# Performance work log

Hardware: AMD Instinct MI355X
Metric: run time of the kernel (lower is better)

## Reference

```python
import jax, jax.numpy as jnp
import numpy as np

B, T, D, L, E = 8, 2048, 256, 8, 64


def setup_inputs() -> dict:
    key = jax.random.key(0)
    ks = jax.random.split(key, 5)
    x = jax.random.normal(ks[0], (B, T, D), dtype=jnp.float32)
    # MMLP params: weight (4L, D, E), bias (4L, E); nn.Linear: (2L, D), (2L,)
    W_ml = jax.random.normal(ks[1], (4 * L, D, E), dtype=jnp.float32) * 0.05
    b_ml = jax.random.normal(ks[2], (4 * L, E), dtype=jnp.float32) * 0.05
    W_lin = jax.random.normal(ks[3], (2 * L, D), dtype=jnp.float32) * 0.05
    b_lin = jax.random.normal(ks[4], (2 * L,), dtype=jnp.float32) * 0.05
    return {"x": x, "W_ml": W_ml, "b_ml": b_ml, "W_lin": W_lin, "b_lin": b_lin}


def _xlstm_forward(x, W_ml, b_ml, W_lin, b_lin):
    b, t, _ = x.shape
    l4, _, e = W_ml.shape
    l = l4 // 4
    # Precompute all per-step gate projections at once (the torch code does this per step).
    mg = jnp.einsum('bti,lij->btlj', x, W_ml) + b_ml          # (B,T,4L,E)
    lg = jnp.einsum('bti,li->btl', x, W_lin) + b_lin          # (B,T,2L)
    o_, v, k, q = jnp.split(mg, 4, axis=2)                    # each (B,T,L,E)
    i_, f_ = jnp.split(lg, 2, axis=2)                         # each (B,T,L)
    xs = tuple(jnp.moveaxis(a, 1, 0) for a in (o_, v, k, q, i_, f_))  # time-major

    def step(carry, inp):
        m, n, C, h = carry
        o_t, v_t, k_t, q_t, i_t, f_t = inp
        m_new = jnp.maximum(f_t + m, i_t)                     # stabilizer (B,L)
        i_g = jnp.exp(i_t - m_new)
        f_g = jnp.exp(f_t + m - m_new)
        # rank-1 outer-product update of matrix cell state (B,L,E,E)
        C = f_g[:, :, None, None] * C + i_g[:, :, None, None] * (v_t[:, :, :, None] * k_t[:, :, None, :])
        n = f_g[:, :, None] * n + i_g[:, :, None] * k_t       # (B,L,E)
        denom = jnp.maximum(jnp.sum(n * q_t, axis=-1), 1.0)[:, :, None]  # clamp(.,1,inf)
        h = jax.nn.sigmoid(o_t) * jnp.einsum('blij,bli->blj', C, q_t) / denom
        return (m_new, n, C, h), None

    init = (
        jnp.zeros((b, l), jnp.float32),
        jnp.zeros((b, l, e), jnp.float32),
        jnp.zeros((b, l, e, e), jnp.float32),
        jnp.zeros((b, l, e), jnp.float32),
    )
    (m, n, C, h), _ = jax.lax.scan(step, init, xs)
    return h, C


def reference(x, W_ml, b_ml, W_lin, b_lin):
    return _xlstm_forward(x, W_ml, b_ml, W_lin, b_lin)
```

## Files before the change

### kernel.cpp

```cpp
#include <hip/hip_runtime.h>

#define B 8
#define T 2048
#define D 256
#define L 8
#define E 64
#define BT (B*T)

typedef _Float16 f16;
typedef f16 f16x8 __attribute__((ext_vector_type(8)));
typedef float f32x4 __attribute__((ext_vector_type(4)));

#define OFF_I   0
#define OFF_F   (OFF_I  + B*L*T)
#define OFF_W16 (OFF_F  + B*L*T)
#define OFF_WT  (OFF_W16 + B*L*T/2)
#define OFF_VT  (OFF_WT + 16*E*D/2)
#define OFF_KT  (OFF_VT + B*L*E*T/2)
#define OFF_CP  (OFF_KT + B*L*E*T/2)
#define OFF_X16 (OFF_CP + 64*4*4160)

__global__ __launch_bounds__(256) void k_prep_x(const float* __restrict__ x,
                                                f16* __restrict__ x16) {
    int i = (blockIdx.x * 256 + threadIdx.x) * 8;
    float4 v0 = *(const float4*)(x + i);
    float4 v1 = *(const float4*)(x + i + 4);
    f16x8 o;
    o[0] = (f16)v0.x; o[1] = (f16)v0.y; o[2] = (f16)v0.z; o[3] = (f16)v0.w;
    o[4] = (f16)v1.x; o[5] = (f16)v1.y; o[6] = (f16)v1.z; o[7] = (f16)v1.w;
    *(f16x8*)(x16 + i) = o;
}

__global__ __launch_bounds__(256) void k_prep(const float* __restrict__ x,
        const float* __restrict__ Wlin, const float* __restrict__ blin,
        const float* __restrict__ Wml,
        float* __restrict__ ibuf, float* __restrict__ fbuf,
        f16* __restrict__ Wt16) {
    __shared__ __align__(16) char smem[49920];
    int tid = threadIdx.x;
    int bx = blockIdx.x;
    if (bx < 512) {
        float (*xs)[260] = (float(*)[260])smem;
        float (*wsm)[260] = (float(*)[260])(smem + 33280);
        int t0 = bx * 32;
        {
            int row = tid >> 3, q = tid & 7;
            const float* src = x + (size_t)(t0 + row) * D + q * 32;
            #pragma unroll
            for (int j = 0; j < 8; ++j) {
                float4 v = *(const float4*)(src + j * 4);
                *(float4*)&xs[row][q * 32 + j * 4] = v;
            }
        }
        {
            int row = tid >> 4, c0 = (tid & 15) * 16;
            const float* src = Wlin + row * D + c0;
            #pragma unroll
            for (int j = 0; j < 4; ++j) {
                float4 v = *(const float4*)(src + j * 4);
                *(float4*)&wsm[row][c0 + j * 4] = v;
            }
        }
        __syncthreads();
        int tl = tid >> 4, g = tid & 15;
        float acc0 = 0.f, acc1 = 0.f;
        for (int i = 0; i < D; ++i) {
            float wv = wsm[g][i];
            acc0 += xs[tl * 2 + 0][i] * wv;
            acc1 += xs[tl * 2 + 1][i] * wv;
        }
        float bias = blin[g];
        float acc[2] = {acc0 + bias, acc1 + bias};
        #pragma unroll
        for (int u = 0; u < 2; ++u) {
            int t = t0 + tl * 2 + u;
            int b = t >> 11, tt = t & 2047;
            if (g < 8) ibuf[(b * L + g) * T + tt] = acc[u];
            else       fbuf[(b * L + (g - 8)) * T + tt] = acc[u];
        }
    } else {
        float (*ts)[65] = (float(*)[65])smem;
        int vkrow = bx - 512;
        int wrow = 8 + vkrow;
        for (int dc = 0; dc < 4; ++dc) {
            int d0 = dc * 64;
            int r = tid >> 2, cq = (tid & 3) * 16;
            const float* src = Wml + ((size_t)wrow * D + d0 + r) * E + cq;
            #pragma unroll
            for (int j = 0; j < 16; j += 4) {
                float4 v = *(const float4*)(src + j);
                ts[r][cq + j] = v.x; ts[r][cq + j + 1] = v.y;
                ts[r][cq + j + 2] = v.z; ts[r][cq + j + 3] = v.w;
            }
            __syncthreads();
            int e = tid >> 2, dq = (tid & 3) * 16;
            f16* dst = Wt16 + ((size_t)vkrow * E + e) * D + d0 + dq;
            f16x8 o0, o1;
            #pragma unroll
            for (int j = 0; j < 8; ++j) {
                o0[j] = (f16)ts[dq + j][e];
                o1[j] = (f16)ts[dq + 8 + j][e];
            }
            *(f16x8*)dst = o0;
            *(f16x8*)(dst + 8) = o1;
            __syncthreads();
        }
    }
}

__global__ __launch_bounds__(256) void k_scan(const float* __restrict__ ibuf,
        const float* __restrict__ fbuf, f16* __restrict__ w16) {
    __shared__ float part[256];
    __shared__ float red[256];
    int tid = threadIdx.x;
    int base = blockIdx.x * T;
    const float* fp = fbuf + base + tid * 8;
    const float* ip = ibuf + base + tid * 8;
    float4 fa = *(const float4*)fp;
    float4 fb = *(const float4*)(fp + 4);
    float4 ia = *(const float4*)ip;
    float4 ib = *(const float4*)(ip + 4);
    float f[8] = {fa.x, fa.y, fa.z, fa.w, fb.x, fb.y, fb.z, fb.w};
    float iv[8] = {ia.x, ia.y, ia.z, ia.w, ib.x, ib.y, ib.z, ib.w};
    float ls[8]; float run = 0.f;
    #pragma unroll
    for (int r = 0; r < 8; ++r) { run += f[r]; ls[r] = run; }
    part[tid] = run;
    __syncthreads();
    float inc = run;
    #pragma unroll
    for (int s = 1; s < 256; s <<= 1) {
        float u = (tid >= s) ? part[tid - s] : 0.f;
        __syncthreads();
        inc += u;
        part[tid] = inc;
        __syncthreads();
    }
    float off = inc - run;
    float e[8]; float lmax = -1e30f;
    #pragma unroll
    for (int r = 0; r < 8; ++r) { e[r] = iv[r] - (off + ls[r]); lmax = fmaxf(lmax, e[r]); }
    red[tid] = lmax;
    __syncthreads();
    for (int s = 128; s > 0; s >>= 1) {
        if (tid < s) red[tid] = fmaxf(red[tid], red[tid + s]);
        __syncthreads();
    }
    float M = fmaxf(red[0], 0.0f);
    f16x8 wv8;
    #pragma unroll
    for (int r = 0; r < 8; ++r) wv8[r] = (f16)__expf(e[r] - M);
    *(f16x8*)(w16 + base + tid * 8) = wv8;
}

__global__ __launch_bounds__(512) void k_vkproj3(const f16* __restrict__ x16,
        const f16* __restrict__ Wt16, const float* __restrict__ bml,
        f16* __restrict__ Vt, f16* __restrict__ Kt) {
    __shared__ __align__(16) char lds[40960];
    int tid = threadIdx.x;
    int bx = blockIdx.x, h = blockIdx.y;
    int t0 = bx * 128;
    const f16* xa = x16 + (size_t)t0 * D;
    const f16* wb = Wt16 + (size_t)h * 8 * E * D;
    int wv = tid >> 6, lane = tid & 63;
    int wr = wv >> 2, wc = wv & 3;
    int q = lane >> 4, lr = lane & 15;
    int sa_t = tid >> 2, sa_q = tid & 3;
    f32x4 acc[4][8] = {};
    for (int ks = 0; ks < 8; ++ks) {
        int k0 = ks * 32;
        {
            f16x8 v = *(const f16x8*)(xa + (size_t)sa_t * D + k0 + sa_q * 8);
            int ba = sa_t * 64 + ((sa_q ^ ((sa_t >> 1) & 3)) << 4);
            *(f16x8*)(lds + ba) = v;
        }
        #pragma unroll
        for (int rr = 0; rr < 4; ++rr) {
            int r = rr * 128 + (tid >> 2);
            int c = tid & 3;
            f16x8 v = *(const f16x8*)(wb + (size_t)r * D + k0 + c * 8);
            int ba = 8192 + r * 64 + ((c ^ ((r >> 1) & 3)) << 4);
            *(f16x8*)(lds + ba) = v;
        }
        __syncthreads();
        f16x8 a[4], bf[8];
        #pragma unroll
        for (int m = 0; m < 4; ++m) {
            int t = wr * 64 + m * 16 + lr;
            int ba = t * 64 + ((q ^ ((t >> 1) & 3)) << 4);
            a[m] = *(const f16x8*)(lds + ba);
        }
        #pragma unroll
        for (int n = 0; n < 8; ++n) {
            int c = wc * 128 + n * 16 + lr;
            int ba = 8192 + c * 64 + ((q ^ ((c >> 1) & 3)) << 4);
            bf[n] = *(const f16x8*)(lds + ba);
        }
        #pragma unroll
        for (int m = 0; m < 4; ++m)
            #pragma unroll
            for (int n = 0; n < 8; ++n)
                acc[m][n] = __builtin_amdgcn_mfma_f32_16x16x32_f16(
                    a[m], bf[n], acc[m][n], 0, 0, 0);
        __syncthreads();
    }
    const float* bp = bml + (size_t)(8 + h * 8) * E;
    int b_g = t0 >> 11, tin = t0 & 2047;
    f16* obase = h ? Kt : Vt;
    for (int p = 0; p < 4; ++p) {
        if (wc == p) {
            #pragma unroll
            for (int n = 0; n < 8; ++n) {
                int cc = n * 16 + lr;
                float bias = bp[p * 128 + cc];
                int swz = (cc & 7) << 4;
                #pragma unroll
                for (int m = 0; m < 4; ++m) {
                    #pragma unroll
                    for (int r = 0; r < 4; r += 2) {
                        int t = wr * 64 + m * 16 + q * 4 + r;
                        union { f16 h2[2]; unsigned u; } pk;
                        pk.h2[0] = (f16)(acc[m][n][r] + bias);
                        pk.h2[1] = (f16)(acc[m][n][r + 1] + bias);
                        int ba = cc * 256 + ((t * 2) ^ swz);
                        *(unsigned*)(lds + ba) = pk.u;
                    }
                }
            }
        }
        __syncthreads();
        {
            int cc = tid >> 2, part = tid & 3;
            int cg = p * 128 + cc;
            int l = cg >> 6, e = cg & 63;
            f16* dst = obase + ((size_t)((b_g * L + l) * E + e)) * T + tin + part * 32;
            int swz = (cc & 7) << 4;
            #pragma unroll
            for (int jj = 0; jj < 4; ++jj) {
                int t = part * 32 + jj * 8;
                int ba = cc * 256 + ((t * 2) ^ swz);
                *(f16x8*)(dst + jj * 8) = *(const f16x8*)(lds + ba);
            }
        }
        __syncthreads();
    }
}

__global__ __launch_bounds__(256) void k_cgemm2(const f16* __restrict__ Vt,
        const f16* __restrict__ Kt, const f16* __restrict__ w16,
        float* __restrict__ Cpart) {
    __shared__ float red[64 * 64];
    __shared__ float redn[64];
    int tid = threadIdx.x;
    int bl = blockIdx.x, tc = blockIdx.y;
    int wv = tid >> 6, lane = tid & 63;
    const f16* vp = Vt + (size_t)bl * E * T;
    const f16* kp = Kt + (size_t)bl * E * T;
    const f16* wp = w16 + (size_t)bl * T;
    f32x4 acc[5][4] = {};
    int tbase = tc * 512 + wv * 128;
    for (int kc = 0; kc < 4; ++kc) {
        int tt = tbase + kc * 32 + (lane >> 4) * 8;
        f16x8 wfrag = *(const f16x8*)(wp + tt);
        f16x8 a[5], bf[4];
        #pragma unroll
        for (int m = 0; m < 4; ++m) {
            int i = m * 16 + (lane & 15);
            f16x8 v = *(const f16x8*)(vp + (size_t)i * T + tt);
            a[m] = v * wfrag;
        }
        a[4] = wfrag;
        #pragma unroll
        for (int nn = 0; nn < 4; ++nn) {
            int j = nn * 16 + (lane & 15);
            bf[nn] = *(const f16x8*)(kp + (size_t)j * T + tt);
        }
        #pragma unroll
        for (int m = 0; m < 5; ++m)
            #pragma unroll
            for (int nn = 0; nn < 4; ++nn)
                acc[m][nn] = __builtin_amdgcn_mfma_f32_16x16x32_f16(
                    a[m], bf[nn], acc[m][nn], 0, 0, 0);
    }
    for (int rr = 0; rr < 4; ++rr) {
        if (wv == rr) {
            #pragma unroll
            for (int m = 0; m < 4; ++m)
                #pragma unroll
                for (int nn = 0; nn < 4; ++nn)
                    #pragma unroll
                    for (int r = 0; r < 4; ++r) {
                        int row = m * 16 + (lane >> 4) * 4 + r;
                        int col = nn * 16 + (lane & 15);
                        if (rr == 0) red[row * 64 + col] = acc[m][nn][r];
                        else         red[row * 64 + col] += acc[m][nn][r];
                    }
            if ((lane >> 4) == 0) {
                #pragma unroll
                for (int nn = 0; nn < 4; ++nn) {
                    int col = nn * 16 + (lane & 15);
                    if (rr == 0) redn[col] = acc[4][nn][0];
                    else         redn[col] += acc[4][nn][0];
                }
            }
        }
        __syncthreads();
    }
    float* cp = Cpart + ((size_t)bl * 4 + tc) * 4160;
    #pragma unroll
    for (int j = 0; j < 4; ++j) {
        int idx = tid * 16 + j * 4;
        *(float4*)(cp + idx) = *(const float4*)(red + idx);
    }
    if (tid < 64) cp[4096 + tid] = redn[tid];
}

__global__ __launch_bounds__(256) void k_final(const float* __restrict__ x,
        const float* __restrict__ Wml, const float* __restrict__ bml,
        const float* __restrict__ Cpart, float* __restrict__ out) {
    __shared__ float Cs[E * E];
    __shared__ float xs[D];
    __shared__ float ns[E];
    __shared__ float os[E];
    __shared__ float qs[E];
    int tid = threadIdx.x;
    int bl = blockIdx.x; int b = bl >> 3, l = bl & 7;
    xs[tid] = x[((size_t)(b * T + (T - 1))) * D + tid];
    const float* cp = Cpart + (size_t)bl * 4 * 4160;
    #pragma unroll
    for (int j = 0; j < 4; ++j) {
        int idx = tid * 16 + j * 4;
        float4 s = {0, 0, 0, 0};
        #pragma unroll
        for (int p = 0; p < 4; ++p) {
            float4 v = *(const float4*)(cp + p * 4160 + idx);
            s.x += v.x; s.y += v.y; s.z += v.z; s.w += v.w;
        }
        *(float4*)&Cs[idx] = s;
        *(float4*)(out + 4096 + (size_t)bl * (E * E) + idx) = s;
    }
    if (tid < 64) {
        float s = 0.f;
        #pragma unroll
        for (int p = 0; p < 4; ++p) s += cp[p * 4160 + 4096 + tid];
        ns[tid] = s;
    }
    __syncthreads();
    if (tid < 128) {
        int gate = tid >> 6, e = tid & 63;
        int wrow = gate ? (3 * L + l) : l;
        const float* wpp = Wml + (size_t)wrow * D * E + e;
        float s = 0.f;
        for (int kk = 0; kk < D; ++kk) s += xs[kk] * wpp[kk * E];
        s += bml[wrow * E + e];
        if (gate) qs[e] = s; else os[e] = s;
    }
    __syncthreads();
    if (tid < 64) {
        int j = tid;
        float hc = 0.f;
        for (int i2 = 0; i2 < E; ++i2) hc += Cs[i2 * E + j] * qs[i2];
        float nq = 0.f;
        for (int i2 = 0; i2 < E; ++i2) nq += ns[i2] * qs[i2];
        float denom = fmaxf(nq, 1.0f);
        float sg = 1.0f / (1.0f + __expf(-os[j]));
        out[bl * E + j] = sg * hc / denom;
    }
}

extern "C" void kernel_launch(void* const* d_in, const int* in_sizes, int n_in,
                              void* d_out, int out_size, void* d_ws, size_t ws_size,
                              hipStream_t stream) {
    const float* x    = (const float*)d_in[0];
    const float* Wml  = (const float*)d_in[1];
    const float* bml  = (const float*)d_in[2];
    const float* Wlin = (const float*)d_in[3];
    const float* blin = (const float*)d_in[4];
    float* out = (float*)d_out;
    float* ws = (float*)d_ws;
    float* ibuf  = ws + OFF_I;
    float* fbuf  = ws + OFF_F;
    f16*   w16   = (f16*)(ws + OFF_W16);
    f16*   Wt16  = (f16*)(ws + OFF_WT);
    f16*   Vt    = (f16*)(ws + OFF_VT);
    f16*   Kt    = (f16*)(ws + OFF_KT);
    float* Cpart = ws + OFF_CP;
    f16*   x16   = (f16*)(ws + OFF_X16);

    k_prep_x<<<BT * D / (256 * 8), 256, 0, stream>>>(x, x16);
    k_prep<<<512 + 16, 256, 0, stream>>>(x, Wlin, blin, Wml, ibuf, fbuf, Wt16);
    k_scan<<<B * L, 256, 0, stream>>>(ibuf, fbuf, w16);
    k_vkproj3<<<dim3(BT / 128, 2), 512, 0, stream>>>(x16, Wt16, bml, Vt, Kt);
    k_cgemm2<<<dim3(B * L, 4), 256, 0, stream>>>(Vt, Kt, w16, Cpart);
    k_final<<<B * L, 256, 0, stream>>>(x, Wml, bml, Cpart, out);
}
```

Measured before the change: 71.39 us.

## Fuse x conversion into prep kernel and gate scan into C-GEMM kernel

Merges the fp32-to-fp16 conversion of x into the prep kernel as extra blocks, and folds the log-space gate scan into the C-GEMM kernel, where each block recomputes the prefix sum and max for its (b,l) row and keeps its slice of weights in LDS. This removes two kernel launches and the global round trip of the weight buffer. In exchange, the scan is computed redundantly by the four time-chunk blocks of each row, and its barrier-heavy prologue now sits in front of the MFMA loop.

Result: faster. 65.34 us, median of 3 (-8.5%).

```diff
diff --git a/kernel.cpp b/kernel.cpp
--- a/kernel.cpp
+++ b/kernel.cpp
@@ -13,29 +13,17 @@
 
 #define OFF_I   0
 #define OFF_F   (OFF_I  + B*L*T)
-#define OFF_W16 (OFF_F  + B*L*T)
-#define OFF_WT  (OFF_W16 + B*L*T/2)
+#define OFF_WT  (OFF_F  + B*L*T)
 #define OFF_VT  (OFF_WT + 16*E*D/2)
 #define OFF_KT  (OFF_VT + B*L*E*T/2)
 #define OFF_CP  (OFF_KT + B*L*E*T/2)
 #define OFF_X16 (OFF_CP + 64*4*4160)
 
-__global__ __launch_bounds__(256) void k_prep_x(const float* __restrict__ x,
-                                                f16* __restrict__ x16) {
-    int i = (blockIdx.x * 256 + threadIdx.x) * 8;
-    float4 v0 = *(const float4*)(x + i);
-    float4 v1 = *(const float4*)(x + i + 4);
-    f16x8 o;
-    o[0] = (f16)v0.x; o[1] = (f16)v0.y; o[2] = (f16)v0.z; o[3] = (f16)v0.w;
-    o[4] = (f16)v1.x; o[5] = (f16)v1.y; o[6] = (f16)v1.z; o[7] = (f16)v1.w;
-    *(f16x8*)(x16 + i) = o;
-}
-
-__global__ __launch_bounds__(256) void k_prep(const float* __restrict__ x,
+__global__ __launch_bounds__(256) void k_prep_all(const float* __restrict__ x,
         const float* __restrict__ Wlin, const float* __restrict__ blin,
         const float* __restrict__ Wml,
         float* __restrict__ ibuf, float* __restrict__ fbuf,
-        f16* __restrict__ Wt16) {
+        f16* __restrict__ Wt16, f16* __restrict__ x16) {
     __shared__ __align__(16) char smem[49920];
     int tid = threadIdx.x;
     int bx = blockIdx.x;
@@ -78,7 +66,7 @@
             if (g < 8) ibuf[(b * L + g) * T + tt] = acc[u];
             else       fbuf[(b * L + (g - 8)) * T + tt] = acc[u];
         }
-    } else {
+    } else if (bx < 528) {
         float (*ts)[65] = (float(*)[65])smem;
         int vkrow = bx - 512;
         int wrow = 8 + vkrow;
@@ -105,52 +93,15 @@
             *(f16x8*)(dst + 8) = o1;
             __syncthreads();
         }
-    }
-}
-
-__global__ __launch_bounds__(256) void k_scan(const float* __restrict__ ibuf,
-        const float* __restrict__ fbuf, f16* __restrict__ w16) {
-    __shared__ float part[256];
-    __shared__ float red[256];
-    int tid = threadIdx.x;
-    int base = blockIdx.x * T;
-    const float* fp = fbuf + base + tid * 8;
-    const float* ip = ibuf + base + tid * 8;
-    float4 fa = *(const float4*)fp;
-    float4 fb = *(const float4*)(fp + 4);
-    float4 ia = *(const float4*)ip;
-    float4 ib = *(const float4*)(ip + 4);
-    float f[8] = {fa.x, fa.y, fa.z, fa.w, fb.x, fb.y, fb.z, fb.w};
-    float iv[8] = {ia.x, ia.y, ia.z, ia.w, ib.x, ib.y, ib.z, ib.w};
-    float ls[8]; float run = 0.f;
-    #pragma unroll
-    for (int r = 0; r < 8; ++r) { run += f[r]; ls[r] = run; }
-    part[tid] = run;
-    __syncthreads();
-    float inc = run;
-    #pragma unroll
-    for (int s = 1; s < 256; s <<= 1) {
-        float u = (tid >= s) ? part[tid - s] : 0.f;
-        __syncthreads();
-        inc += u;
-        part[tid] = inc;
-        __syncthreads();
-    }
-    float off = inc - run;
-    float e[8]; float lmax = -1e30f;
-    #pragma unroll
-    for (int r = 0; r < 8; ++r) { e[r] = iv[r] - (off + ls[r]); lmax = fmaxf(lmax, e[r]); }
-    red[tid] = lmax;
-    __syncthreads();
-    for (int s = 128; s > 0; s >>= 1) {
-        if (tid < s) red[tid] = fmaxf(red[tid], red[tid + s]);
-        __syncthreads();
-    }
-    float M = fmaxf(red[0], 0.0f);
-    f16x8 wv8;
-    #pragma unroll
-    for (int r = 0; r < 8; ++r) wv8[r] = (f16)__expf(e[r] - M);
-    *(f16x8*)(w16 + base + tid * 8) = wv8;
+    } else {
+        int i = ((bx - 528) * 256 + tid) * 8;
+        float4 v0 = *(const float4*)(x + i);
+        float4 v1 = *(const float4*)(x + i + 4);
+        f16x8 o;
+        o[0] = (f16)v0.x; o[1] = (f16)v0.y; o[2] = (f16)v0.z; o[3] = (f16)v0.w;
+        o[4] = (f16)v1.x; o[5] = (f16)v1.y; o[6] = (f16)v1.z; o[7] = (f16)v1.w;
+        *(f16x8*)(x16 + i) = o;
+    }
 }
 
 __global__ __launch_bounds__(512) void k_vkproj3(const f16* __restrict__ x16,
@@ -246,22 +197,67 @@
     }
 }
 
-__global__ __launch_bounds__(256) void k_cgemm2(const f16* __restrict__ Vt,
-        const f16* __restrict__ Kt, const f16* __restrict__ w16,
-        float* __restrict__ Cpart) {
+__global__ __launch_bounds__(256) void k_cgemm2s(const f16* __restrict__ Vt,
+        const f16* __restrict__ Kt, const float* __restrict__ ibuf,
+        const float* __restrict__ fbuf, float* __restrict__ Cpart) {
     __shared__ float red[64 * 64];
     __shared__ float redn[64];
+    __shared__ float part[256];
+    __shared__ float rmax[256];
+    __shared__ __align__(16) f16 wlds[512];
     int tid = threadIdx.x;
     int bl = blockIdx.x, tc = blockIdx.y;
     int wv = tid >> 6, lane = tid & 63;
+    {
+        const float* fp = fbuf + bl * T + tid * 8;
+        const float* ip = ibuf + bl * T + tid * 8;
+        float4 fa = *(const float4*)fp;
+        float4 fb = *(const float4*)(fp + 4);
+        float4 ia = *(const float4*)ip;
+        float4 ib = *(const float4*)(ip + 4);
+        float f[8] = {fa.x, fa.y, fa.z, fa.w, fb.x, fb.y, fb.z, fb.w};
+        float iv[8] = {ia.x, ia.y, ia.z, ia.w, ib.x, ib.y, ib.z, ib.w};
+        float ls[8]; float run = 0.f;
+        #pragma unroll
+        for (int r = 0; r < 8; ++r) { run += f[r]; ls[r] = run; }
+        part[tid] = run;
+        __syncthreads();
+        float inc = run;
+        #pragma unroll
+        for (int s = 1; s < 256; s <<= 1) {
+            float u = (tid >= s) ? part[tid - s] : 0.f;
+            __syncthreads();
+            inc += u;
+            part[tid] = inc;
+            __syncthreads();
+        }
+        float off = inc - run;
+        float e[8]; float lmax = -1e30f;
+        #pragma unroll
+        for (int r = 0; r < 8; ++r) { e[r] = iv[r] - (off + ls[r]); lmax = fmaxf(lmax, e[r]); }
+        rmax[tid] = lmax;
+        __syncthreads();
+        for (int s = 128; s > 0; s >>= 1) {
+            if (tid < s) rmax[tid] = fmaxf(rmax[tid], rmax[tid + s]);
+            __syncthreads();
+        }
+        float M = fmaxf(rmax[0], 0.0f);
+        int t = tid * 8;
+        if ((t >> 9) == tc) {
+            f16x8 w8;
+            #pragma unroll
+            for (int r = 0; r < 8; ++r) w8[r] = (f16)__expf(e[r] - M);
+            *(f16x8*)&wlds[t & 511] = w8;
+        }
+        __syncthreads();
+    }
     const f16* vp = Vt + (size_t)bl * E * T;
     const f16* kp = Kt + (size_t)bl * E * T;
-    const f16* wp = w16 + (size_t)bl * T;
     f32x4 acc[5][4] = {};
     int tbase = tc * 512 + wv * 128;
     for (int kc = 0; kc < 4; ++kc) {
         int tt = tbase + kc * 32 + (lane >> 4) * 8;
-        f16x8 wfrag = *(const f16x8*)(wp + tt);
+        f16x8 wfrag = *(const f16x8*)&wlds[tt & 511];
         f16x8 a[5], bf[4];
         #pragma unroll
         for (int m = 0; m < 4; ++m) {
@@ -380,17 +376,14 @@
     float* ws = (float*)d_ws;
     float* ibuf  = ws + OFF_I;
     float* fbuf  = ws + OFF_F;
-    f16*   w16   = (f16*)(ws + OFF_W16);
     f16*   Wt16  = (f16*)(ws + OFF_WT);
     f16*   Vt    = (f16*)(ws + OFF_VT);
     f16*   Kt    = (f16*)(ws + OFF_KT);
     float* Cpart = ws + OFF_CP;
     f16*   x16   = (f16*)(ws + OFF_X16);
 
-    k_prep_x<<<BT * D / (256 * 8), 256, 0, stream>>>(x, x16);
-    k_prep<<<512 + 16, 256, 0, stream>>>(x, Wlin, blin, Wml, ibuf, fbuf, Wt16);
-    k_scan<<<B * L, 256, 0, stream>>>(ibuf, fbuf, w16);
+    k_prep_all<<<2576, 256, 0, stream>>>(x, Wlin, blin, Wml, ibuf, fbuf, Wt16, x16);
     k_vkproj3<<<dim3(BT / 128, 2), 512, 0, stream>>>(x16, Wt16, bml, Vt, Kt);
-    k_cgemm2<<<dim3(B * L, 4), 256, 0, stream>>>(Vt, Kt, w16, Cpart);
+    k_cgemm2s<<<dim3(B * L, 4), 256, 0, stream>>>(Vt, Kt, ibuf, fbuf, Cpart);
     k_final<<<B * L, 256, 0, stream>>>(x, Wml, bml, Cpart, out);
 }
```
